# Kernel optimization log

Hardware: AMD Instinct MI355X
Metric: run time of the kernel (lower is better)

The kernel has to match this reference:

```python
import jax, jax.numpy as jnp
import numpy as np

B, K, D, L, POS = 128, 128, 512, 2, 64
DI = 2 * D           # d_inner = dim * expand(2)
HH, WW = 64, 64
GS = 16              # hilbert grid_size


def _ln(x, g, b):
    m = jnp.mean(x, axis=-1, keepdims=True)
    v = jnp.mean(jnp.square(x - m), axis=-1, keepdims=True)
    return (x - m) * jax.lax.rsqrt(v + 1e-5) * g + b


def _ssm(x, g, b, wi, bi, wo, bo):
    # LinearAttentionSSM: x + proj_out(silu(z) * sigmoid(gate)) with z,gate = proj_in(LN(x)).chunk(2)
    h = _ln(x, g, b) @ wi + bi
    z, gate = jnp.split(h, 2, axis=-1)
    return x + (jax.nn.silu(z) * jax.nn.sigmoid(gate)) @ wo + bo


def _hilbert_d(x, y, n=GS):
    # vectorized xy2d_hilbert over arbitrary int arrays
    d = jnp.zeros_like(x)
    s = n // 2
    while s > 0:
        rx = ((x & s) > 0).astype(jnp.int32)
        ry = ((y & s) > 0).astype(jnp.int32)
        d = d + s * s * jnp.bitwise_xor(3 * rx, ry)
        x, y = (jnp.where(ry == 0, jnp.where(rx == 1, s - 1 - y, y), x),
                jnp.where(ry == 0, jnp.where(rx == 1, s - 1 - x, x), y))
        s //= 2
    return d


def _forward(H, W, slots, keep_mask, attn_maps,
             pm1_w, pm1_b, pm2_w, pm2_b,
             fwd_ln_g, fwd_ln_b, fwd_in_w, fwd_in_b, fwd_out_w, fwd_out_b,
             bwd_ln_g, bwd_ln_b, bwd_in_w, bwd_in_b, bwd_out_w, bwd_out_b,
             merge_w, merge_b, norm_g, norm_b,
             ffn_ln_g, ffn_ln_b, ffn1_w, ffn1_b, ffn2_w, ffn2_b):
    Bz, Kz, Dz = slots.shape
    dt = slots.dtype
    # ---- SlotSpatialEncoder ----
    gy = jnp.arange(H, dtype=dt) / max(H - 1, 1)
    gx = jnp.arange(W, dtype=dt) / max(W - 1, 1)
    grid_y, grid_x = jnp.meshgrid(gy, gx, indexing='ij')
    coords = jnp.stack([grid_x.ravel(), grid_y.ravel()], axis=-1)       # [N,2]
    ap = attn_maps[:, :Kz, :]
    ap = ap / (ap.sum(axis=-1, keepdims=True) + 1e-8)
    centroids = jnp.einsum('bkn,nc->bkc', ap, coords)                   # [B,K,2]
    feats = jnp.concatenate([centroids, jnp.full_like(centroids, 0.1)], axis=-1)  # [B,K,4]
    freqs = 1.0 / (10000.0 ** (jnp.arange(0, POS, 2, dtype=jnp.float32) / POS))
    angles = feats[..., None] * freqs * 3.14159                         # [B,K,4,POS//2]
    enc = jnp.concatenate([jnp.sin(angles), jnp.cos(angles)], axis=-1).reshape(Bz, Kz, 4 * POS)
    pos_enc = jax.nn.gelu(enc @ pm1_w + pm1_b, approximate=False) @ pm2_w + pm2_b
    slots = slots + pos_enc
    # ---- Hilbert ordering (same centroids => same order each layer) ----
    cx = jnp.clip(centroids[..., 0] * (GS - 1), 0, GS - 1).astype(jnp.int32)
    cy = jnp.clip(centroids[..., 1] * (GS - 1), 0, GS - 1).astype(jnp.int32)
    order = jnp.argsort(_hilbert_d(cx, cy), axis=-1)                    # [B,K]
    reverse = jnp.argsort(order, axis=-1)
    # ---- layers ----
    for i in range(L):
        residual = slots
        ordered = jnp.take_along_axis(slots, order[..., None], axis=1)
        f = _ssm(ordered, fwd_ln_g[i], fwd_ln_b[i], fwd_in_w[i], fwd_in_b[i], fwd_out_w[i], fwd_out_b[i])
        bk = _ssm(ordered[:, ::-1], bwd_ln_g[i], bwd_ln_b[i], bwd_in_w[i], bwd_in_b[i], bwd_out_w[i], bwd_out_b[i])[:, ::-1]
        merged = jnp.concatenate([f, bk], axis=-1) @ merge_w[i] + merge_b[i]
        unord = jnp.take_along_axis(merged, reverse[..., None], axis=1)
        slots = _ln(residual + unord, norm_g[i], norm_b[i])
        ff = jax.nn.gelu(_ln(slots, ffn_ln_g[i], ffn_ln_b[i]) @ ffn1_w[i] + ffn1_b[i], approximate=False) @ ffn2_w[i] + ffn2_b[i]
        slots = slots + ff
        slots = slots * keep_mask[..., None]
    return slots, centroids


def setup_inputs() -> dict:
    key = jax.random.key(0)
    ks = iter(jax.random.split(key, 32))
    w = lambda *s: jax.random.normal(next(ks), s, jnp.float32) * 0.02
    z = lambda *s: jnp.zeros(s, jnp.float32)
    o = lambda *s: jnp.ones(s, jnp.float32)
    return {
        'slots': jax.random.normal(next(ks), (B, K, D), jnp.float32),
        'keep_mask': o(B, K),
        'attn_maps': jax.random.uniform(next(ks), (B, K, HH * WW), jnp.float32),
        'H': HH, 'W': WW,
        'pm1_w': w(4 * POS, D), 'pm1_b': z(D), 'pm2_w': w(D, D), 'pm2_b': z(D),
        'fwd_ln_g': o(L, D), 'fwd_ln_b': z(L, D),
        'fwd_in_w': w(L, D, 2 * DI), 'fwd_in_b': z(L, 2 * DI),
        'fwd_out_w': w(L, DI, D), 'fwd_out_b': z(L, D),
        'bwd_ln_g': o(L, D), 'bwd_ln_b': z(L, D),
        'bwd_in_w': w(L, D, 2 * DI), 'bwd_in_b': z(L, 2 * DI),
        'bwd_out_w': w(L, DI, D), 'bwd_out_b': z(L, D),
        'merge_w': w(L, 2 * D, D), 'merge_b': z(L, D),
        'norm_g': o(L, D), 'norm_b': z(L, D),
        'ffn_ln_g': o(L, D), 'ffn_ln_b': z(L, D),
        'ffn1_w': w(L, D, 4 * D), 'ffn1_b': z(L, 4 * D),
        'ffn2_w': w(L, 4 * D, D), 'ffn2_b': z(L, D),
    }


def reference(slots, keep_mask, attn_maps, H, W,
              pm1_w, pm1_b, pm2_w, pm2_b,
              fwd_ln_g, fwd_ln_b, fwd_in_w, fwd_in_b, fwd_out_w, fwd_out_b,
              bwd_ln_g, bwd_ln_b, bwd_in_w, bwd_in_b, bwd_out_w, bwd_out_b,
              merge_w, merge_b, norm_g, norm_b,
              ffn_ln_g, ffn_ln_b, ffn1_w, ffn1_b, ffn2_w, ffn2_b):
    return _forward(H, W, slots, keep_mask, attn_maps,
                    pm1_w, pm1_b, pm2_w, pm2_b,
                    fwd_ln_g, fwd_ln_b, fwd_in_w, fwd_in_b, fwd_out_w, fwd_out_b,
                    bwd_ln_g, bwd_ln_b, bwd_in_w, bwd_in_b, bwd_out_w, bwd_out_b,
                    merge_w, merge_b, norm_g, norm_b,
                    ffn_ln_g, ffn_ln_b, ffn1_w, ffn1_b, ffn2_w, ffn2_b)
```

## Files before the change

### kernel.cpp

```cpp
#include <hip/hip_runtime.h>

typedef __bf16 bf16_t;
typedef __bf16 bf16x8 __attribute__((ext_vector_type(8)));
typedef __bf16 bf16x4 __attribute__((ext_vector_type(4)));
typedef float  f32x4  __attribute__((ext_vector_type(4)));

#define MODE_GELU   0
#define MODE_GATED  1
#define MODE_RES_F  3
#define MODE_FFN2   4
#define MODE_STORE  5

__device__ __forceinline__ void async16(const void* g, void* l) {
  __builtin_amdgcn_global_load_lds(
      (const __attribute__((address_space(1))) void*)g,
      (__attribute__((address_space(3))) void*)l, 16, 0, 0);
}

__device__ __forceinline__ float fast_exp(float x) {
  return __builtin_amdgcn_exp2f(x * 1.44269504088896f);
}
__device__ __forceinline__ float fast_sigmoid(float x) {
  return __builtin_amdgcn_rcpf(1.0f + fast_exp(-x));
}
__device__ __forceinline__ float fast_gelu(float x) {
  float u = fabsf(x) * 0.70710678118f;
  float t = __builtin_amdgcn_rcpf(fmaf(0.3275911f, u, 1.0f));
  float p = t * fmaf(t, fmaf(t, fmaf(t, fmaf(t, 1.061405429f, -1.453152027f),
                                     1.421413741f), -0.284496736f), 0.254829592f);
  float e = __builtin_amdgcn_exp2f(-u * u * 1.44269504088896f);
  float erfu = fmaf(-p, e, 1.0f);
  float s = (x >= 0.f) ? erfu : -erfu;
  return 0.5f * x * (1.0f + s);
}

template<int MODE>
__launch_bounds__(256, (MODE == MODE_GATED) ? 2 : 3)
__global__ void gemm_mfma(const bf16_t* __restrict__ A,
                          const bf16_t* __restrict__ B1,
                          const bf16_t* __restrict__ B2,
                          const float*  __restrict__ bias,
                          const float*  __restrict__ Xres,
                          const float*  __restrict__ mask,
                          void* __restrict__ Cptr,
                          int M, int N, int K, int lda, int ldC, int coff)
{
  constexpr bool DUAL = (MODE == MODE_GATED);
  __shared__ bf16_t sA[128 * 64];
  __shared__ bf16_t sB[128 * 64];
  __shared__ bf16_t sB2[DUAL ? 128 * 64 : 8];

  const int tid  = threadIdx.x;
  const int wave = tid >> 6;
  const int lane = tid & 63;
  const int wm = wave & 1;
  const int wn = wave >> 1;
  const long m0 = (long)blockIdx.y * 128;
  const long n0 = (long)blockIdx.x * 128;

  f32x4 zero4 = {0.f, 0.f, 0.f, 0.f};
  f32x4 acc[4][4];
  f32x4 acc2[DUAL ? 4 : 1][DUAL ? 4 : 1];
#pragma unroll
  for (int i = 0; i < 4; i++)
#pragma unroll
    for (int j = 0; j < 4; j++) acc[i][j] = zero4;
  if constexpr (DUAL) {
#pragma unroll
    for (int i = 0; i < 4; i++)
#pragma unroll
      for (int j = 0; j < 4; j++) acc2[i][j] = zero4;
  }

  const int q    = lane >> 4;
  const int c16  = lane & 15;
  const int sr   = lane >> 3;
  const int sg   = lane & 7;
  const int stRow = wave * 8 + sr;

  for (long k0 = 0; k0 < K; k0 += 64) {
#pragma unroll
    for (int i = 0; i < 4; i++) {
      int  r     = i * 32 + stRow;
      int  g     = sg ^ (r & 7);
      long gA    = (long)r * lda + k0 + g * 8;
      long gB    = (long)r * K   + k0 + g * 8;
      int  lbase = i * 2048 + wave * 512;
      async16(A  + m0 * lda + gA, &sA[lbase]);
      async16(B1 + n0 * K   + gB, &sB[lbase]);
      if constexpr (DUAL) async16(B2 + n0 * K + gB, &sB2[lbase]);
    }
    __syncthreads();
#pragma unroll
    for (int kk = 0; kk < 2; kk++) {
      bf16x8 af[4], bfr[4], b2fr[DUAL ? 4 : 1];
#pragma unroll
      for (int i = 0; i < 4; i++) {
        int r = wm * 64 + i * 16 + c16;
        int g = (kk * 4 + q) ^ (r & 7);
        af[i] = *(const bf16x8*)&sA[r * 64 + g * 8];
      }
#pragma unroll
      for (int j = 0; j < 4; j++) {
        int r = wn * 64 + j * 16 + c16;
        int g = (kk * 4 + q) ^ (r & 7);
        bfr[j] = *(const bf16x8*)&sB[r * 64 + g * 8];
        if constexpr (DUAL) b2fr[j] = *(const bf16x8*)&sB2[r * 64 + g * 8];
      }
#pragma unroll
      for (int i = 0; i < 4; i++)
#pragma unroll
        for (int j = 0; j < 4; j++) {
          acc[i][j] = __builtin_amdgcn_mfma_f32_16x16x32_bf16(af[i], bfr[j], acc[i][j], 0, 0, 0);
          if constexpr (DUAL)
            acc2[i][j] = __builtin_amdgcn_mfma_f32_16x16x32_bf16(af[i], b2fr[j], acc2[i][j], 0, 0, 0);
        }
    }
    __syncthreads();
  }

#pragma unroll
  for (int i = 0; i < 4; i++) {
#pragma unroll
    for (int j = 0; j < 4; j++) {
#pragma unroll
      for (int r = 0; r < 4; r++) {
        long m = m0 + wm * 64 + i * 16 + q * 4 + r;
        long n = n0 + wn * 64 + j * 16 + c16;
        float v = acc[i][j][r];
        if constexpr (MODE == MODE_GELU) {
          float x  = v + bias[n];
          ((bf16_t*)Cptr)[m * (long)ldC + n] = (bf16_t)fast_gelu(x);
        } else if constexpr (MODE == MODE_GATED) {
          float z  = v + bias[n];
          float gt = acc2[i][j][r] + bias[N + n];
          float sz = z * fast_sigmoid(z);
          float sg_ = fast_sigmoid(gt);
          ((bf16_t*)Cptr)[m * (long)ldC + n] = (bf16_t)(sz * sg_);
        } else if constexpr (MODE == MODE_RES_F) {
          float x = Xres[m * (long)N + n] + v + bias[n];
          ((float*)Cptr)[m * (long)ldC + n] = x;
        } else if constexpr (MODE == MODE_FFN2) {
          float x = (Xres[m * (long)N + n] + v + bias[n]) * mask[m];
          ((float*)Cptr)[m * (long)ldC + n] = x;
        } else {
          ((bf16_t*)Cptr)[m * (long)ldC + coff + n] = (bf16_t)v;
        }
      }
    }
  }
}

struct TransDesc { const float* src; bf16_t* dst; const float* rowScale;
                   int K, ncols, srcLd, srcColOff, tileBase, mode; };
struct TransArgs { TransDesc d[24]; int nd; };

__global__ void transpose_all(TransArgs args) {
  __shared__ float tile[32][33];
  int bid = blockIdx.x;
  int di = 0;
  while (di + 1 < args.nd && bid >= args.d[di + 1].tileBase) ++di;
  TransDesc d = args.d[di];
  int t = bid - d.tileBase;
  if (d.mode == 1) {
    long idx = (long)t * 1024 + threadIdx.x * 4;
    float4 v = *(const float4*)(d.src + idx);
    bf16x4 o; o[0] = (bf16_t)v.x; o[1] = (bf16_t)v.y; o[2] = (bf16_t)v.z; o[3] = (bf16_t)v.w;
    *(bf16x4*)(d.dst + idx) = o;
    return;
  }
  int tilesX = d.ncols >> 5;
  int ty = t / tilesX, tx = t % tilesX;
  int lx = threadIdx.x & 31, ly = threadIdx.x >> 5;
  int gx = tx * 32 + lx;
#pragma unroll
  for (int i = 0; i < 32; i += 8) {
    int gy = ty * 32 + ly + i;
    float sc = d.rowScale ? d.rowScale[gy] : 1.f;
    tile[ly + i][lx] = d.src[(long)gy * d.srcLd + d.srcColOff + gx] * sc;
  }
  __syncthreads();
  int ox = ty * 32 + lx;
#pragma unroll
  for (int i = 0; i < 32; i += 8) {
    int oy = tx * 32 + ly + i;
    d.dst[(long)oy * d.K + ox] = (bf16_t)tile[lx][ly + i];
  }
}

struct GemvDesc { const float* v; const float* W; const float* b0; float* out;
                  int K, ldW, colOff, jBase, N; };
struct GemvArgs { GemvDesc d[12]; int nd; };

__global__ void gemv_all(GemvArgs a) {
  int j = blockIdx.x * 256 + threadIdx.x;
  int di = 0;
  while (di + 1 < a.nd && j >= a.d[di + 1].jBase) ++di;
  GemvDesc d = a.d[di];
  int jj = j - d.jBase;
  if (jj >= d.N) return;
  float s = d.b0 ? d.b0[jj] : 0.f;
  for (int k = 0; k < d.K; k++) s += d.v[k] * d.W[(long)k * d.ldW + d.colOff + jj];
  d.out[jj] = s;
}

__global__ void bias_u_kernel(const float* __restrict__ fob, const float* __restrict__ bob,
                              const float* __restrict__ mw, const float* __restrict__ mb,
                              float* __restrict__ out) {
  int n = blockIdx.x * 256 + threadIdx.x;
  float s = mb[n];
  for (int k = 0; k < 512; k++)
    s += fob[k] * mw[k * 512 + n] + bob[k] * mw[(512 + k) * 512 + n];
  out[n] = s;
}

__global__ void build_mtmb(const bf16_t* __restrict__ mt0, bf16_t* __restrict__ bc0,
                           const bf16_t* __restrict__ mt1, bf16_t* __restrict__ bc1) {
  int idx = blockIdx.x * 256 + threadIdx.x;
  int l = idx >> 18;
  int r = idx & 262143;
  int n = r >> 9, k = r & 511;
  const bf16_t* mt = l ? mt1 : mt0;
  bf16_t* bc = l ? bc1 : bc0;
  float v = (float)mt[n * 1024 + k] + (float)mt[n * 1024 + 512 + k];
  bc[(long)n * 2560 + 2048 + k] = (bf16_t)v;
}

__global__ void centroid_kernel(const float* __restrict__ attn,
                                float* __restrict__ cent,
                                float* __restrict__ outCent) {
  int wave = threadIdx.x >> 6, lane = threadIdx.x & 63;
  long row = (long)blockIdx.x * 4 + wave;
  const float4* ap = (const float4*)(attn + row * 4096);
  float s = 0.f, sx = 0.f, sy = 0.f;
#pragma unroll 4
  for (int t = 0; t < 16; t++) {
    float4 v = ap[t * 64 + lane];
    int n0 = (t * 64 + lane) * 4;
    float col = (float)(n0 & 63);
    float ry  = (float)(n0 >> 6);
    float rs = v.x + v.y + v.z + v.w;
    s  += rs;
    sx += v.x * col + v.y * (col + 1.f) + v.z * (col + 2.f) + v.w * (col + 3.f);
    sy += rs * ry;
  }
#pragma unroll
  for (int o = 32; o; o >>= 1) {
    s += __shfl_down(s, o); sx += __shfl_down(sx, o); sy += __shfl_down(sy, o);
  }
  if (lane == 0) {
    float denom = s + 1e-8f;
    float cx = (sx * (1.f / 63.f)) / denom;
    float cy = (sy * (1.f / 63.f)) / denom;
    cent[row * 2] = cx;     cent[row * 2 + 1] = cy;
    outCent[row * 2] = cx;  outCent[row * 2 + 1] = cy;
  }
}

__global__ void enc_kernel(const float* __restrict__ cent, bf16_t* __restrict__ enc) {
  int tid = blockIdx.x * 256 + threadIdx.x;
  int row = tid >> 5, j = tid & 31;
  float cx = cent[row * 2], cy = cent[row * 2 + 1];
  float freq = expf(-(float)j * 0.28782313662425572f);
  float fx = cx * freq * 3.14159f;
  float fy = cy * freq * 3.14159f;
  float fc = 0.1f * freq * 3.14159f;
  bf16_t* e = enc + (long)row * 256;
  float sc = sinf(fc), cc = cosf(fc);
  e[j]        = (bf16_t)sinf(fx);  e[32 + j]  = (bf16_t)cosf(fx);
  e[64 + j]   = (bf16_t)sinf(fy);  e[96 + j]  = (bf16_t)cosf(fy);
  e[128 + j]  = (bf16_t)sc;        e[160 + j] = (bf16_t)cc;
  e[192 + j]  = (bf16_t)sc;        e[224 + j] = (bf16_t)cc;
}

__global__ void ln_plain_kernel(const float* __restrict__ X,
                                bf16_t* __restrict__ Xn, bf16_t* __restrict__ Sx) {
  int wave = threadIdx.x >> 6, lane = threadIdx.x & 63;
  long row = (long)blockIdx.x * 4 + wave;
  const float4* xp = (const float4*)(X + row * 512);
  float4 v0 = xp[lane], v1 = xp[64 + lane];
  float s  = v0.x + v0.y + v0.z + v0.w + v1.x + v1.y + v1.z + v1.w;
  float s2 = v0.x*v0.x + v0.y*v0.y + v0.z*v0.z + v0.w*v0.w
           + v1.x*v1.x + v1.y*v1.y + v1.z*v1.z + v1.w*v1.w;
#pragma unroll
  for (int o = 32; o; o >>= 1) { s += __shfl_xor(s, o); s2 += __shfl_xor(s2, o); }
  float mean = s * (1.f / 512.f);
  float var  = s2 * (1.f / 512.f) - mean * mean;
  float rstd = rsqrtf(var + 1e-5f);
  float xs[8] = {v0.x, v0.y, v0.z, v0.w, v1.x, v1.y, v1.z, v1.w};
  int   c0 = lane * 4, c1 = 256 + lane * 4;
  bf16x4 pa, pr;
#pragma unroll
  for (int t = 0; t < 4; t++) {
    pa[t] = (bf16_t)((xs[t] - mean) * rstd);
    pr[t] = (bf16_t)xs[t];
  }
  *(bf16x4*)&Xn[row * 512 + c0] = pa;
  *(bf16x4*)&Sx[row * 2560 + c0] = pr;
#pragma unroll
  for (int t = 0; t < 4; t++) {
    pa[t] = (bf16_t)((xs[4 + t] - mean) * rstd);
    pr[t] = (bf16_t)xs[4 + t];
  }
  *(bf16x4*)&Xn[row * 512 + c1] = pa;
  *(bf16x4*)&Sx[row * 2560 + c1] = pr;
}

__global__ void ln_dual_kernel(const float* __restrict__ U,
                               const float* __restrict__ ng, const float* __restrict__ nb,
                               float* __restrict__ Y, bf16_t* __restrict__ Yln) {
  int wave = threadIdx.x >> 6, lane = threadIdx.x & 63;
  long row = (long)blockIdx.x * 4 + wave;
  const float4* xp = (const float4*)(U + row * 512);
  float4 v0 = xp[lane], v1 = xp[64 + lane];
  float s  = v0.x + v0.y + v0.z + v0.w + v1.x + v1.y + v1.z + v1.w;
  float s2 = v0.x*v0.x + v0.y*v0.y + v0.z*v0.z + v0.w*v0.w
           + v1.x*v1.x + v1.y*v1.y + v1.z*v1.z + v1.w*v1.w;
#pragma unroll
  for (int o = 32; o; o >>= 1) { s += __shfl_xor(s, o); s2 += __shfl_xor(s2, o); }
  float mean = s * (1.f / 512.f);
  float var  = s2 * (1.f / 512.f) - mean * mean;
  float rstd = rsqrtf(var + 1e-5f);
  float xs[8] = {v0.x, v0.y, v0.z, v0.w, v1.x, v1.y, v1.z, v1.w};
  int   c0 = lane * 4, c1 = 256 + lane * 4;
  float y[8];
#pragma unroll
  for (int t = 0; t < 4; t++) y[t]     = (xs[t] - mean) * rstd * ng[c0 + t] + nb[c0 + t];
#pragma unroll
  for (int t = 0; t < 4; t++) y[4 + t] = (xs[4 + t] - mean) * rstd * ng[c1 + t] + nb[c1 + t];
  float4 w0 = {y[0], y[1], y[2], y[3]}, w1 = {y[4], y[5], y[6], y[7]};
  float4* yp = (float4*)(Y + row * 512);
  yp[lane] = w0; yp[64 + lane] = w1;
  float t1 = 0.f, t2 = 0.f;
#pragma unroll
  for (int t = 0; t < 8; t++) { t1 += y[t]; t2 += y[t] * y[t]; }
#pragma unroll
  for (int o = 32; o; o >>= 1) { t1 += __shfl_xor(t1, o); t2 += __shfl_xor(t2, o); }
  float mean2 = t1 * (1.f / 512.f);
  float var2  = t2 * (1.f / 512.f) - mean2 * mean2;
  float rstd2 = rsqrtf(var2 + 1e-5f);
  bf16x4 pa;
#pragma unroll
  for (int t = 0; t < 4; t++) pa[t] = (bf16_t)((y[t] - mean2) * rstd2);
  *(bf16x4*)&Yln[row * 512 + c0] = pa;
#pragma unroll
  for (int t = 0; t < 4; t++) pa[t] = (bf16_t)((y[4 + t] - mean2) * rstd2);
  *(bf16x4*)&Yln[row * 512 + c1] = pa;
}

extern "C" void kernel_launch(void* const* d_in, const int* in_sizes, int n_in,
                              void* d_out, int out_size, void* d_ws, size_t ws_size,
                              hipStream_t stream) {
  const int M = 16384;
  const float* slots    = (const float*)d_in[0];
  const float* keep     = (const float*)d_in[1];
  const float* attn     = (const float*)d_in[2];
  const float* pm1_w    = (const float*)d_in[5];
  const float* pm1_b    = (const float*)d_in[6];
  const float* pm2_w    = (const float*)d_in[7];
  const float* pm2_b    = (const float*)d_in[8];
  const float* fwd_ln_g = (const float*)d_in[9];
  const float* fwd_ln_b = (const float*)d_in[10];
  const float* fwd_in_w = (const float*)d_in[11];
  const float* fwd_in_b = (const float*)d_in[12];
  const float* fwd_out_w= (const float*)d_in[13];
  const float* fwd_out_b= (const float*)d_in[14];
  const float* bwd_ln_g = (const float*)d_in[15];
  const float* bwd_ln_b = (const float*)d_in[16];
  const float* bwd_in_w = (const float*)d_in[17];
  const float* bwd_in_b = (const float*)d_in[18];
  const float* bwd_out_w= (const float*)d_in[19];
  const float* bwd_out_b= (const float*)d_in[20];
  const float* merge_w  = (const float*)d_in[21];
  const float* merge_b  = (const float*)d_in[22];
  const float* norm_g   = (const float*)d_in[23];
  const float* norm_b   = (const float*)d_in[24];
  const float* ffn_ln_g = (const float*)d_in[25];
  const float* ffn_ln_b = (const float*)d_in[26];
  const float* ffn1_w   = (const float*)d_in[27];
  const float* ffn1_b   = (const float*)d_in[28];
  const float* ffn2_w   = (const float*)d_in[29];
  const float* ffn2_b   = (const float*)d_in[30];

  char* w = (char*)d_ws;
  size_t off = 0;
  auto alloc = [&](size_t bytes) { size_t r = off; off += (bytes + 255) & ~(size_t)255; return r; };

  bf16_t* pm1t = (bf16_t*)(w + alloc(512 * 256 * 2));
  bf16_t* pm2t = (bf16_t*)(w + alloc(512 * 512 * 2));
  bf16_t *WzT[2], *WgT[2], *ffn1t[2], *ffn2t[2], *merget[2], *foutbf[2], *boutbf[2], *Bcomp[2];
  float  *bias_gated[2], *bias_ffn1[2], *bias_u[2];
  for (int l = 0; l < 2; l++) {
    WzT[l]    = (bf16_t*)(w + alloc(2048 * 512 * 2));
    WgT[l]    = (bf16_t*)(w + alloc(2048 * 512 * 2));
    ffn1t[l]  = (bf16_t*)(w + alloc(2048 * 512 * 2));
    ffn2t[l]  = (bf16_t*)(w + alloc(512 * 2048 * 2));
    merget[l] = (bf16_t*)(w + alloc(512 * 1024 * 2));
    foutbf[l] = (bf16_t*)(w + alloc(1024 * 512 * 2));
    boutbf[l] = (bf16_t*)(w + alloc(1024 * 512 * 2));
    Bcomp[l]  = (bf16_t*)(w + alloc(512 * 2560 * 2));
    bias_gated[l] = (float*)(w + alloc(4096 * 4));
    bias_ffn1[l]  = (float*)(w + alloc(2048 * 4));
    bias_u[l]     = (float*)(w + alloc(512 * 4));
  }
  float*  cent = (float*)(w + alloc((size_t)M * 2 * 4));
  float*  X    = (float*)(w + alloc((size_t)M * 512 * 4));
  float*  Y    = (float*)(w + alloc((size_t)M * 512 * 4));
  float*  U    = (float*)(w + alloc((size_t)M * 512 * 4));
  bf16_t* Xn   = (bf16_t*)(w + alloc((size_t)M * 512 * 2));
  bf16_t* S    = (bf16_t*)(w + alloc((size_t)M * 2560 * 2));
  bf16_t* FF1  = (bf16_t*)(w + alloc((size_t)M * 2048 * 2));
  bf16_t* Yln  = (bf16_t*)(w + alloc((size_t)M * 512 * 2));
  bf16_t* Enc  = (bf16_t*)(w + alloc((size_t)M * 256 * 2));
  bf16_t* P1   = (bf16_t*)(w + alloc((size_t)M * 512 * 2));

  const size_t WSTRIDE = (size_t)512 * 2048;

  TransArgs ta{};
  int nt = 0, tb = 0;
  auto addT = [&](const float* s, bf16_t* dst, const float* scale,
                  int K, int ncols, int srcLd, int srcColOff, int mode) {
    ta.d[nt] = {s, dst, scale, K, ncols, srcLd, srcColOff, tb, mode};
    tb += (K * ncols) >> 10; nt++;
  };
  addT(pm1_w, pm1t, nullptr, 256, 512, 512, 0, 0);
  addT(pm2_w, pm2t, nullptr, 512, 512, 512, 0, 0);
  for (int l = 0; l < 2; l++) {
    const float* fiw = fwd_in_w + (size_t)l * WSTRIDE;
    const float* biw = bwd_in_w + (size_t)l * WSTRIDE;
    addT(fiw, WzT[l],               fwd_ln_g + l * 512, 512, 1024, 2048, 0,    0);
    addT(biw, WzT[l] + 1024 * 512,  bwd_ln_g + l * 512, 512, 1024, 2048, 0,    0);
    addT(fiw, WgT[l],               fwd_ln_g + l * 512, 512, 1024, 2048, 1024, 0);
    addT(biw, WgT[l] + 1024 * 512,  bwd_ln_g + l * 512, 512, 1024, 2048, 1024, 0);
    addT(merge_w + (size_t)l * 1024 * 512, merget[l], nullptr, 1024, 512, 512, 0, 0);
    addT(ffn1_w + (size_t)l * WSTRIDE, ffn1t[l], ffn_ln_g + l * 512, 512, 2048, 2048, 0, 0);
    addT(ffn2_w + (size_t)l * WSTRIDE, ffn2t[l], nullptr, 2048, 512, 512, 0, 0);
    addT(fwd_out_w + (size_t)l * 1024 * 512, foutbf[l], nullptr, 1024, 512, 0, 0, 1);
    addT(bwd_out_w + (size_t)l * 1024 * 512, boutbf[l], nullptr, 1024, 512, 0, 0, 1);
  }
  ta.nd = nt;
  transpose_all<<<tb, 256, 0, stream>>>(ta);

  for (int l = 0; l < 2; l++) {
    gemm_mfma<MODE_STORE><<<dim3(8, 4), 256, 0, stream>>>(
        merget[l], foutbf[l], nullptr, nullptr, nullptr, nullptr,
        Bcomp[l], 512, 1024, 512, 1024, 2560, 0);
    gemm_mfma<MODE_STORE><<<dim3(8, 4), 256, 0, stream>>>(
        merget[l] + 512, boutbf[l], nullptr, nullptr, nullptr, nullptr,
        Bcomp[l], 512, 1024, 512, 1024, 2560, 1024);
  }
  build_mtmb<<<2048, 256, 0, stream>>>(merget[0], Bcomp[0], merget[1], Bcomp[1]);

  GemvArgs ga{};
  int ng_ = 0, jb = 0;
  auto addG = [&](const float* v, const float* W, const float* b0, float* out,
                  int K, int ldW, int colOff, int N) {
    ga.d[ng_] = {v, W, b0, out, K, ldW, colOff, jb, N};
    jb += N; ng_++;
  };
  for (int l = 0; l < 2; l++) {
    const float* fiw = fwd_in_w + (size_t)l * WSTRIDE;
    const float* biw = bwd_in_w + (size_t)l * WSTRIDE;
    addG(fwd_ln_b + l * 512, fiw, fwd_in_b + l * 2048,        bias_gated[l],        512, 2048, 0,    1024);
    addG(bwd_ln_b + l * 512, biw, bwd_in_b + l * 2048,        bias_gated[l] + 1024, 512, 2048, 0,    1024);
    addG(fwd_ln_b + l * 512, fiw, fwd_in_b + l * 2048 + 1024, bias_gated[l] + 2048, 512, 2048, 1024, 1024);
    addG(bwd_ln_b + l * 512, biw, bwd_in_b + l * 2048 + 1024, bias_gated[l] + 3072, 512, 2048, 1024, 1024);
    addG(ffn_ln_b + l * 512, ffn1_w + (size_t)l * WSTRIDE, ffn1_b + l * 2048, bias_ffn1[l], 512, 2048, 0, 2048);
  }
  ga.nd = ng_;
  gemv_all<<<jb / 256, 256, 0, stream>>>(ga);
  for (int l = 0; l < 2; l++)
    bias_u_kernel<<<2, 256, 0, stream>>>(fwd_out_b + l * 512, bwd_out_b + l * 512,
                                         merge_w + (size_t)l * 1024 * 512,
                                         merge_b + l * 512, bias_u[l]);

  float* outCent = (float*)d_out + (size_t)M * 512;
  centroid_kernel<<<M / 4, 256, 0, stream>>>(attn, cent, outCent);
  enc_kernel<<<(M * 32) / 256, 256, 0, stream>>>(cent, Enc);

  gemm_mfma<MODE_GELU><<<dim3(4, 128), 256, 0, stream>>>(
      Enc, pm1t, nullptr, pm1_b, nullptr, nullptr, P1, M, 512, 256, 256, 512, 0);
  gemm_mfma<MODE_RES_F><<<dim3(4, 128), 256, 0, stream>>>(
      P1, pm2t, nullptr, pm2_b, slots, nullptr, X, M, 512, 512, 512, 512, 0);

  for (int l = 0; l < 2; l++) {
    ln_plain_kernel<<<M / 4, 256, 0, stream>>>(X, Xn, S + 2048);
    gemm_mfma<MODE_GATED><<<dim3(16, 128), 256, 0, stream>>>(
        Xn, WzT[l], WgT[l], bias_gated[l], nullptr, nullptr, S,
        M, 2048, 512, 512, 2560, 0);
    gemm_mfma<MODE_RES_F><<<dim3(4, 128), 256, 0, stream>>>(
        S, Bcomp[l], nullptr, bias_u[l], X, nullptr, U,
        M, 512, 2560, 2560, 512, 0);
    ln_dual_kernel<<<M / 4, 256, 0, stream>>>(U, norm_g + l * 512, norm_b + l * 512, Y, Yln);
    gemm_mfma<MODE_GELU><<<dim3(16, 128), 256, 0, stream>>>(
        Yln, ffn1t[l], nullptr, bias_ffn1[l], nullptr, nullptr, FF1,
        M, 2048, 512, 512, 2048, 0);
    float* Xdst = (l == 1) ? (float*)d_out : X;
    gemm_mfma<MODE_FFN2><<<dim3(4, 128), 256, 0, stream>>>(
        FF1, ffn2t[l], nullptr, ffn2_b + l * 512, Y, keep, Xdst,
        M, 512, 2048, 2048, 512, 0);
  }
}
```

Measured before the change: 1.315 ms.

## Fold bias GEMVs into weight transpose and batch prep GEMMs into one launch

```diff
diff --git a/kernel.cpp b/kernel.cpp
--- a/kernel.cpp
+++ b/kernel.cpp
@@ -9,7 +9,6 @@
 #define MODE_GATED  1
 #define MODE_RES_F  3
 #define MODE_FFN2   4
-#define MODE_STORE  5
 
 __device__ __forceinline__ void async16(const void* g, void* l) {
   __builtin_amdgcn_global_load_lds(
@@ -140,23 +139,101 @@
         } else if constexpr (MODE == MODE_RES_F) {
           float x = Xres[m * (long)N + n] + v + bias[n];
           ((float*)Cptr)[m * (long)ldC + n] = x;
-        } else if constexpr (MODE == MODE_FFN2) {
+        } else {
           float x = (Xres[m * (long)N + n] + v + bias[n]) * mask[m];
           ((float*)Cptr)[m * (long)ldC + n] = x;
-        } else {
-          ((bf16_t*)Cptr)[m * (long)ldC + coff + n] = (bf16_t)v;
         }
       }
     }
   }
 }
 
+struct PrepDesc { const bf16_t* A; const bf16_t* B; bf16_t* C; int coff; };
+struct PrepArgs { PrepDesc d[4]; };
+
+__launch_bounds__(256, 3)
+__global__ void gemm_prep_all(PrepArgs a) {
+  PrepDesc d = a.d[blockIdx.x >> 5];
+  const int t = blockIdx.x & 31;
+  const long m0 = (long)(t >> 3) * 128;
+  const long n0 = (long)(t & 7) * 128;
+  const int lda = 1024, K = 512, ldC = 2560;
+
+  __shared__ bf16_t sA[128 * 64];
+  __shared__ bf16_t sB[128 * 64];
+
+  const int tid  = threadIdx.x;
+  const int wave = tid >> 6;
+  const int lane = tid & 63;
+  const int wm = wave & 1;
+  const int wn = wave >> 1;
+
+  f32x4 zero4 = {0.f, 0.f, 0.f, 0.f};
+  f32x4 acc[4][4];
+#pragma unroll
+  for (int i = 0; i < 4; i++)
+#pragma unroll
+    for (int j = 0; j < 4; j++) acc[i][j] = zero4;
+
+  const int q    = lane >> 4;
+  const int c16  = lane & 15;
+  const int sr   = lane >> 3;
+  const int sg   = lane & 7;
+  const int stRow = wave * 8 + sr;
+
+  for (long k0 = 0; k0 < K; k0 += 64) {
+#pragma unroll
+    for (int i = 0; i < 4; i++) {
+      int  r     = i * 32 + stRow;
+      int  g     = sg ^ (r & 7);
+      int  lbase = i * 2048 + wave * 512;
+      async16(d.A + (m0 + r) * lda + k0 + g * 8, &sA[lbase]);
+      async16(d.B + (n0 + r) * K   + k0 + g * 8, &sB[lbase]);
+    }
+    __syncthreads();
+#pragma unroll
+    for (int kk = 0; kk < 2; kk++) {
+      bf16x8 af[4], bfr[4];
+#pragma unroll
+      for (int i = 0; i < 4; i++) {
+        int r = wm * 64 + i * 16 + c16;
+        int g = (kk * 4 + q) ^ (r & 7);
+        af[i] = *(const bf16x8*)&sA[r * 64 + g * 8];
+      }
+#pragma unroll
+      for (int j = 0; j < 4; j++) {
+        int r = wn * 64 + j * 16 + c16;
+        int g = (kk * 4 + q) ^ (r & 7);
+        bfr[j] = *(const bf16x8*)&sB[r * 64 + g * 8];
+      }
+#pragma unroll
+      for (int i = 0; i < 4; i++)
+#pragma unroll
+        for (int j = 0; j < 4; j++)
+          acc[i][j] = __builtin_amdgcn_mfma_f32_16x16x32_bf16(af[i], bfr[j], acc[i][j], 0, 0, 0);
+    }
+    __syncthreads();
+  }
+#pragma unroll
+  for (int i = 0; i < 4; i++)
+#pragma unroll
+    for (int j = 0; j < 4; j++)
+#pragma unroll
+      for (int r = 0; r < 4; r++) {
+        long m = m0 + wm * 64 + i * 16 + q * 4 + r;
+        long n = n0 + wn * 64 + j * 16 + c16;
+        d.C[m * ldC + d.coff + n] = (bf16_t)acc[i][j][r];
+      }
+}
+
 struct TransDesc { const float* src; bf16_t* dst; const float* rowScale;
+                   const float* accVa; const float* accVb; float* accOut;
                    int K, ncols, srcLd, srcColOff, tileBase, mode; };
 struct TransArgs { TransDesc d[24]; int nd; };
 
 __global__ void transpose_all(TransArgs args) {
   __shared__ float tile[32][33];
+  __shared__ float red[8][32];
   int bid = blockIdx.x;
   int di = 0;
   while (di + 1 < args.nd && bid >= args.d[di + 1].tileBase) ++di;
@@ -173,13 +250,26 @@
   int ty = t / tilesX, tx = t % tilesX;
   int lx = threadIdx.x & 31, ly = threadIdx.x >> 5;
   int gx = tx * 32 + lx;
+  float p = 0.f;
 #pragma unroll
   for (int i = 0; i < 32; i += 8) {
     int gy = ty * 32 + ly + i;
+    float raw = d.src[(long)gy * d.srcLd + d.srcColOff + gx];
+    if (d.accOut) {
+      float v = (d.accVb && gy >= 512) ? d.accVb[gy - 512] : d.accVa[gy];
+      p += v * raw;
+    }
     float sc = d.rowScale ? d.rowScale[gy] : 1.f;
-    tile[ly + i][lx] = d.src[(long)gy * d.srcLd + d.srcColOff + gx] * sc;
-  }
+    tile[ly + i][lx] = raw * sc;
+  }
+  if (d.accOut) red[ly][lx] = p;
   __syncthreads();
+  if (d.accOut && ly == 0) {
+    float s = 0.f;
+#pragma unroll
+    for (int r = 0; r < 8; r++) s += red[r][lx];
+    atomicAdd(&d.accOut[tx * 32 + lx], s);
+  }
   int ox = ty * 32 + lx;
 #pragma unroll
   for (int i = 0; i < 32; i += 8) {
@@ -188,30 +278,15 @@
   }
 }
 
-struct GemvDesc { const float* v; const float* W; const float* b0; float* out;
-                  int K, ldW, colOff, jBase, N; };
-struct GemvArgs { GemvDesc d[12]; int nd; };
-
-__global__ void gemv_all(GemvArgs a) {
-  int j = blockIdx.x * 256 + threadIdx.x;
+struct CopyDesc { const float* src; float* dst; int base, len; };
+struct CopyArgs { CopyDesc d[12]; int nd; };
+__global__ void init_bias(CopyArgs a) {
+  int i = blockIdx.x * 256 + threadIdx.x;
   int di = 0;
-  while (di + 1 < a.nd && j >= a.d[di + 1].jBase) ++di;
-  GemvDesc d = a.d[di];
-  int jj = j - d.jBase;
-  if (jj >= d.N) return;
-  float s = d.b0 ? d.b0[jj] : 0.f;
-  for (int k = 0; k < d.K; k++) s += d.v[k] * d.W[(long)k * d.ldW + d.colOff + jj];
-  d.out[jj] = s;
-}
-
-__global__ void bias_u_kernel(const float* __restrict__ fob, const float* __restrict__ bob,
-                              const float* __restrict__ mw, const float* __restrict__ mb,
-                              float* __restrict__ out) {
-  int n = blockIdx.x * 256 + threadIdx.x;
-  float s = mb[n];
-  for (int k = 0; k < 512; k++)
-    s += fob[k] * mw[k * 512 + n] + bob[k] * mw[(512 + k) * 512 + n];
-  out[n] = s;
+  while (di + 1 < a.nd && i >= a.d[di + 1].base) ++di;
+  CopyDesc d = a.d[di];
+  int j = i - d.base;
+  if (j < d.len) d.dst[j] = d.src[j];
 }
 
 __global__ void build_mtmb(const bf16_t* __restrict__ mt0, bf16_t* __restrict__ bc0,
@@ -416,63 +491,60 @@
 
   const size_t WSTRIDE = (size_t)512 * 2048;
 
+  CopyArgs ca{};
+  int nc = 0, cb = 0;
+  auto addC = [&](const float* s, float* dst, int len) {
+    ca.d[nc] = {s, dst, cb, len};
+    cb += (len + 255) & ~255; nc++;
+  };
+  for (int l = 0; l < 2; l++) {
+    addC(fwd_in_b + l * 2048,        bias_gated[l],        1024);
+    addC(bwd_in_b + l * 2048,        bias_gated[l] + 1024, 1024);
+    addC(fwd_in_b + l * 2048 + 1024, bias_gated[l] + 2048, 1024);
+    addC(bwd_in_b + l * 2048 + 1024, bias_gated[l] + 3072, 1024);
+    addC(ffn1_b + l * 2048,          bias_ffn1[l],         2048);
+    addC(merge_b + l * 512,          bias_u[l],            512);
+  }
+  ca.nd = nc;
+  init_bias<<<cb / 256, 256, 0, stream>>>(ca);
+
   TransArgs ta{};
   int nt = 0, tb = 0;
   auto addT = [&](const float* s, bf16_t* dst, const float* scale,
+                  const float* va, const float* vb, float* accOut,
                   int K, int ncols, int srcLd, int srcColOff, int mode) {
-    ta.d[nt] = {s, dst, scale, K, ncols, srcLd, srcColOff, tb, mode};
+    ta.d[nt] = {s, dst, scale, va, vb, accOut, K, ncols, srcLd, srcColOff, tb, mode};
     tb += (K * ncols) >> 10; nt++;
   };
-  addT(pm1_w, pm1t, nullptr, 256, 512, 512, 0, 0);
-  addT(pm2_w, pm2t, nullptr, 512, 512, 512, 0, 0);
+  addT(pm1_w, pm1t, nullptr, nullptr, nullptr, nullptr, 256, 512, 512, 0, 0);
+  addT(pm2_w, pm2t, nullptr, nullptr, nullptr, nullptr, 512, 512, 512, 0, 0);
   for (int l = 0; l < 2; l++) {
     const float* fiw = fwd_in_w + (size_t)l * WSTRIDE;
     const float* biw = bwd_in_w + (size_t)l * WSTRIDE;
-    addT(fiw, WzT[l],               fwd_ln_g + l * 512, 512, 1024, 2048, 0,    0);
-    addT(biw, WzT[l] + 1024 * 512,  bwd_ln_g + l * 512, 512, 1024, 2048, 0,    0);
-    addT(fiw, WgT[l],               fwd_ln_g + l * 512, 512, 1024, 2048, 1024, 0);
-    addT(biw, WgT[l] + 1024 * 512,  bwd_ln_g + l * 512, 512, 1024, 2048, 1024, 0);
-    addT(merge_w + (size_t)l * 1024 * 512, merget[l], nullptr, 1024, 512, 512, 0, 0);
-    addT(ffn1_w + (size_t)l * WSTRIDE, ffn1t[l], ffn_ln_g + l * 512, 512, 2048, 2048, 0, 0);
-    addT(ffn2_w + (size_t)l * WSTRIDE, ffn2t[l], nullptr, 2048, 512, 512, 0, 0);
-    addT(fwd_out_w + (size_t)l * 1024 * 512, foutbf[l], nullptr, 1024, 512, 0, 0, 1);
-    addT(bwd_out_w + (size_t)l * 1024 * 512, boutbf[l], nullptr, 1024, 512, 0, 0, 1);
+    const float* flb = fwd_ln_b + l * 512;
+    const float* blb = bwd_ln_b + l * 512;
+    addT(fiw, WzT[l],              fwd_ln_g + l * 512, flb, nullptr, bias_gated[l],        512, 1024, 2048, 0,    0);
+    addT(biw, WzT[l] + 1024 * 512, bwd_ln_g + l * 512, blb, nullptr, bias_gated[l] + 1024, 512, 1024, 2048, 0,    0);
+    addT(fiw, WgT[l],              fwd_ln_g + l * 512, flb, nullptr, bias_gated[l] + 2048, 512, 1024, 2048, 1024, 0);
+    addT(biw, WgT[l] + 1024 * 512, bwd_ln_g + l * 512, blb, nullptr, bias_gated[l] + 3072, 512, 1024, 2048, 1024, 0);
+    addT(merge_w + (size_t)l * 1024 * 512, merget[l], nullptr,
+         fwd_out_b + l * 512, bwd_out_b + l * 512, bias_u[l], 1024, 512, 512, 0, 0);
+    addT(ffn1_w + (size_t)l * WSTRIDE, ffn1t[l], ffn_ln_g + l * 512,
+         ffn_ln_b + l * 512, nullptr, bias_ffn1[l], 512, 2048, 2048, 0, 0);
+    addT(ffn2_w + (size_t)l * WSTRIDE, ffn2t[l], nullptr, nullptr, nullptr, nullptr, 2048, 512, 512, 0, 0);
+    addT(fwd_out_w + (size_t)l * 1024 * 512, foutbf[l], nullptr, nullptr, nullptr, nullptr, 1024, 512, 0, 0, 1);
+    addT(bwd_out_w + (size_t)l * 1024 * 512, boutbf[l], nullptr, nullptr, nullptr, nullptr, 1024, 512, 0, 0, 1);
   }
   ta.nd = nt;
   transpose_all<<<tb, 256, 0, stream>>>(ta);
 
-  for (int l = 0; l < 2; l++) {
-    gemm_mfma<MODE_STORE><<<dim3(8, 4), 256, 0, stream>>>(
-        merget[l], foutbf[l], nullptr, nullptr, nullptr, nullptr,
-        Bcomp[l], 512, 1024, 512, 1024, 2560, 0);
-    gemm_mfma<MODE_STORE><<<dim3(8, 4), 256, 0, stream>>>(
-        merget[l] + 512, boutbf[l], nullptr, nullptr, nullptr, nullptr,
-        Bcomp[l], 512, 1024, 512, 1024, 2560, 1024);
-  }
+  PrepArgs pa{};
+  pa.d[0] = {merget[0],       foutbf[0], Bcomp[0], 0};
+  pa.d[1] = {merget[0] + 512, boutbf[0], Bcomp[0], 1024};
+  pa.d[2] = {merget[1],       foutbf[1], Bcomp[1], 0};
+  pa.d[3] = {merget[1] + 512, boutbf[1], Bcomp[1], 1024};
+  gemm_prep_all<<<128, 256, 0, stream>>>(pa);
   build_mtmb<<<2048, 256, 0, stream>>>(merget[0], Bcomp[0], merget[1], Bcomp[1]);
-
-  GemvArgs ga{};
-  int ng_ = 0, jb = 0;
-  auto addG = [&](const float* v, const float* W, const float* b0, float* out,
-                  int K, int ldW, int colOff, int N) {
-    ga.d[ng_] = {v, W, b0, out, K, ldW, colOff, jb, N};
-    jb += N; ng_++;
-  };
-  for (int l = 0; l < 2; l++) {
-    const float* fiw = fwd_in_w + (size_t)l * WSTRIDE;
-    const float* biw = bwd_in_w + (size_t)l * WSTRIDE;
-    addG(fwd_ln_b + l * 512, fiw, fwd_in_b + l * 2048,        bias_gated[l],        512, 2048, 0,    1024);
-    addG(bwd_ln_b + l * 512, biw, bwd_in_b + l * 2048,        bias_gated[l] + 1024, 512, 2048, 0,    1024);
-    addG(fwd_ln_b + l * 512, fiw, fwd_in_b + l * 2048 + 1024, bias_gated[l] + 2048, 512, 2048, 1024, 1024);
-    addG(bwd_ln_b + l * 512, biw, bwd_in_b + l * 2048 + 1024, bias_gated[l] + 3072, 512, 2048, 1024, 1024);
-    addG(ffn_ln_b + l * 512, ffn1_w + (size_t)l * WSTRIDE, ffn1_b + l * 2048, bias_ffn1[l], 512, 2048, 0, 2048);
-  }
-  ga.nd = ng_;
-  gemv_all<<<jb / 256, 256, 0, stream>>>(ga);
-  for (int l = 0; l < 2; l++)
-    bias_u_kernel<<<2, 256, 0, stream>>>(fwd_out_b + l * 512, bwd_out_b + l * 512,
-                                         merge_w + (size_t)l * 1024 * 512,
-                                         merge_b + l * 512, bias_u[l]);
 
   float* outCent = (float*)d_out + (size_t)M * 512;
   centroid_kernel<<<M / 4, 256, 0, stream>>>(attn, cent, outCent);
```

After: 1.113 ms. 1.18x faster.
